# Performance work log

Measured on AMD Instinct MI355X. Metric: run time of the kernel, lower is better.

## Reference

```python
import jax, jax.numpy as jnp
import numpy as np

NUM_KERNELS = 5


def setup_inputs() -> dict:
    key = jax.random.key(0)
    k1, k2 = jax.random.split(key)
    B, D = 4096, 256
    return {
        "s_feat": jax.random.normal(k1, (B, D), dtype=jnp.float32),
        "t_feat": jax.random.normal(k2, (B, D), dtype=jnp.float32),
    }


def _pairwise_sq_dists(feats):
    # Gram-matrix form of sum((x_i - x_j)**2, axis=-1); same math as the
    # broadcasted (x - y)**2 sum, without the [N, N, D] intermediate.
    sq = jnp.sum(feats * feats, axis=-1)  # [N]
    d = sq[:, None] + sq[None, :] - 2.0 * (feats @ feats.T)  # [N, N]
    return jnp.maximum(d, 0.0)


def reference(s_feat, t_feat):
    batch = s_feat.shape[0]
    feats = jnp.concatenate((s_feat, t_feat), axis=0)  # [2B, D]
    distances = _pairwise_sq_dists(feats)  # [2B, 2B]

    # Median-heuristic-style bandwidth (detached in original).
    n = 2 * batch
    bandwidth = float(n * n - n) / jnp.sum(jax.lax.stop_gradient(distances))
    bandwidth = bandwidth / (2 ** (NUM_KERNELS // 2))
    gammas = [bandwidth * (2 ** i) for i in range(NUM_KERNELS)]

    # Multi-gamma Gaussian kernel average (fixed small loop over kernels).
    kern = sum(jnp.exp(-distances * g) for g in gammas) / NUM_KERNELS

    s2s = kern[:batch, :batch]
    t2t = kern[batch:, batch:]
    s2t = kern[:batch, batch:]
    disc = jnp.mean(s2s + t2t - 2.0 * s2t)
    return disc
```

## Files before the change

### kernel.cpp

```cpp
#include <hip/hip_runtime.h>
#include <stdint.h>
#include <math.h>

#define BATCH 4096
#define NT    8192
#define FD    256
#define TILE  128
#define BK    32
#define NUMK  5

typedef __attribute__((ext_vector_type(8))) short bf16x8;
typedef __attribute__((ext_vector_type(4))) float f32x4;

static const size_t WS_FB    = 0;
static const size_t WS_SQ    = (size_t)NT * FD * 2;
static const size_t WS_COL   = WS_SQ + (size_t)NT * 4;
static const size_t WS_SUMSQ = WS_COL + 256 * 4;

__device__ __forceinline__ unsigned short f2bf_rne(float x) {
    unsigned u = __float_as_uint(x);
    unsigned r = (u + 0x7fffu + ((u >> 16) & 1u)) >> 16;
    return (unsigned short)r;
}

__device__ __forceinline__ void async_copy16(void* lds, const void* g) {
    __builtin_amdgcn_global_load_lds(
        (__attribute__((address_space(1))) void*)(void*)(const_cast<void*>(g)),
        (__attribute__((address_space(3))) void*)lds, 16, 0, 0);
}

__global__ void mmd_prep(const float* __restrict__ s_feat,
                         const float* __restrict__ t_feat,
                         unsigned short* __restrict__ fb,
                         float* __restrict__ sq,
                         float* __restrict__ colsum,
                         float* __restrict__ sumsq,
                         float* __restrict__ out) {
    __shared__ float cp[4][FD];
    if (blockIdx.x == 0 && threadIdx.x == 0) atomicExch(out, 0.0f);
    const int w    = threadIdx.x >> 6;
    const int lane = threadIdx.x & 63;
    float c0 = 0.f, c1 = 0.f, c2 = 0.f, c3 = 0.f;
    float wtot = 0.f;
    for (int t = 0; t < 8; ++t) {
        int row = blockIdx.x * 32 + w * 8 + t;
        const float* src = (row < BATCH) ? (s_feat + (size_t)row * FD)
                                         : (t_feat + (size_t)(row - BATCH) * FD);
        float4 v = ((const float4*)src)[lane];
        unsigned int u01 = (unsigned)f2bf_rne(v.x) | ((unsigned)f2bf_rne(v.y) << 16);
        unsigned int u23 = (unsigned)f2bf_rne(v.z) | ((unsigned)f2bf_rne(v.w) << 16);
        ((uint2*)(fb + (size_t)row * FD))[lane] = make_uint2(u01, u23);
        float ss = v.x * v.x + v.y * v.y + v.z * v.z + v.w * v.w;
        for (int off = 32; off; off >>= 1) ss += __shfl_down(ss, off);
        if (lane == 0) { sq[row] = ss; wtot += ss; }
        c0 += v.x; c1 += v.y; c2 += v.z; c3 += v.w;
    }
    if (lane == 0) atomicAdd(sumsq, wtot);
    cp[w][4 * lane + 0] = c0;
    cp[w][4 * lane + 1] = c1;
    cp[w][4 * lane + 2] = c2;
    cp[w][4 * lane + 3] = c3;
    __syncthreads();
    int t = threadIdx.x;
    float s = cp[0][t] + cp[1][t] + cp[2][t] + cp[3][t];
    atomicAdd(&colsum[t], s);
}

__global__ __launch_bounds__(256, 4) void mmd_main(
    const unsigned short* __restrict__ fb,
    const float* __restrict__ sq,
    const float* __restrict__ colsum,
    const float* __restrict__ sumsq,
    float* __restrict__ out) {
    const int bid = blockIdx.x;
    int r = (int)((sqrtf(8.0f * (float)bid + 1.0f) - 1.0f) * 0.5f);
    while ((r + 1) * (r + 2) / 2 <= bid) ++r;
    while (r * (r + 1) / 2 > bid) --r;
    const int bi = bid - r * (r + 1) / 2;
    const int bj = r;

    __shared__ __align__(16) unsigned short a_t[3][TILE * BK];
    __shared__ __align__(16) unsigned short b_t[3][TILE * BK];
    __shared__ float sqa[TILE], sqb[TILE];
    __shared__ float red[4];

    const int tid  = threadIdx.x;
    const int w    = tid >> 6, lane = tid & 63;
    const int wm   = w & 1, wn = w >> 1;
    const int quad = lane >> 4, m16 = lane & 15;
    const int lrow16 = lane >> 2;
    const int pslot  = lane & 3;

    const size_t rowA0 = (size_t)bi * TILE;
    const size_t rowB0 = (size_t)bj * TILE;

#define STAGE(buf, k0_) do {                                                   \
        _Pragma("unroll")                                                      \
        for (int q = 0; q < 2; ++q) {                                          \
            int rr = w * 32 + q * 16 + lrow16;                                 \
            int gcq = pslot ^ ((rr >> 1) & 3);                                 \
            async_copy16(&a_t[buf][(w * 32 + q * 16) * BK],                    \
                         fb + (rowA0 + rr) * FD + (k0_) + gcq * 8);            \
        }                                                                      \
        _Pragma("unroll")                                                      \
        for (int q = 0; q < 2; ++q) {                                          \
            int rr = w * 32 + q * 16 + lrow16;                                 \
            int gcq = pslot ^ ((rr >> 1) & 3);                                 \
            async_copy16(&b_t[buf][(w * 32 + q * 16) * BK],                    \
                         fb + (rowB0 + rr) * FD + (k0_) + gcq * 8);            \
        }                                                                      \
    } while (0)

    STAGE(0, 0);
    STAGE(1, BK);

    float4 c4 = ((const float4*)colsum)[lane];
    float cv = c4.x * c4.x + c4.y * c4.y + c4.z * c4.z + c4.w * c4.w;
    for (int off = 1; off < 64; off <<= 1) cv += __shfl_xor(cv, off);
    const float sumd = 2.0f * (float)NT * sumsq[0] - 2.0f * cv;
    const float n2n  = (float)((long long)NT * NT - NT);
    const float g0   = 0.25f * (n2n / sumd);

    if (tid < TILE) sqa[tid] = sq[bi * TILE + tid];
    else            sqb[tid - TILE] = sq[bj * TILE + (tid - TILE)];

    const f32x4 fzero = {0.f, 0.f, 0.f, 0.f};
    f32x4 acc[4][4];
#pragma unroll
    for (int a = 0; a < 4; ++a)
#pragma unroll
        for (int b = 0; b < 4; ++b) acc[a][b] = fzero;

    __syncthreads();

#pragma unroll
    for (int st = 0; st < 8; ++st) {
        if (st >= 2) {
            if (st == 7) asm volatile("s_waitcnt vmcnt(0)" ::: "memory");
            else         asm volatile("s_waitcnt vmcnt(4)" ::: "memory");
        }
        if (st > 0) {
            __builtin_amdgcn_s_barrier();
            __builtin_amdgcn_sched_barrier(0);
        }
        const int cur = st % 3;

        bf16x8 af[4], bf[4];
#pragma unroll
        for (int tm = 0; tm < 4; ++tm) {
            int row = wm * 64 + tm * 16 + m16;
            int p = quad ^ ((row >> 1) & 3);
            af[tm] = *(const bf16x8*)&a_t[cur][row * BK + p * 8];
        }
#pragma unroll
        for (int tn = 0; tn < 4; ++tn) {
            int row = wn * 64 + tn * 16 + m16;
            int p = quad ^ ((row >> 1) & 3);
            bf[tn] = *(const bf16x8*)&b_t[cur][row * BK + p * 8];
        }

        if (st < 6) STAGE((st + 2) % 3, (st + 2) * BK);

        __builtin_amdgcn_s_setprio(1);
#pragma unroll
        for (int tm = 0; tm < 4; ++tm)
#pragma unroll
            for (int tn = 0; tn < 4; ++tn)
                acc[tm][tn] = __builtin_amdgcn_mfma_f32_16x16x32_bf16(
                    af[tm], bf[tn], acc[tm][tn], 0, 0, 0);
        __builtin_amdgcn_s_setprio(0);
    }

    float lsum = 0.f;
#pragma unroll
    for (int tm = 0; tm < 4; ++tm) {
        const int i0 = wm * 64 + tm * 16 + quad * 4;
        float sqi0 = sqa[i0 + 0], sqi1 = sqa[i0 + 1], sqi2 = sqa[i0 + 2], sqi3 = sqa[i0 + 3];
#pragma unroll
        for (int tn = 0; tn < 4; ++tn) {
            const int j = wn * 64 + tn * 16 + m16;
            const float sqj = sqb[j];
            float sqi[4] = {sqi0, sqi1, sqi2, sqi3};
#pragma unroll
            for (int rr = 0; rr < 4; ++rr) {
                float d = fmaf(-2.f, acc[tm][tn][rr], sqi[rr] + sqj);
                d = fmaxf(d, 0.f);
                float e1 = __expf(-d * g0);
                float e2 = e1 * e1, e4 = e2 * e2, e8 = e4 * e4, e16 = e8 * e8;
                lsum += e1 + e2 + e4 + e8 + e16;
            }
        }
    }
    for (int off = 32; off; off >>= 1) lsum += __shfl_down(lsum, off);
    if (lane == 0) red[w] = lsum;
    __syncthreads();
    if (tid == 0) {
        float wgt;
        if (bi == bj) wgt = 1.f;
        else wgt = ((bi < 32) == (bj < 32)) ? 2.f : -2.f;
        float scale = wgt * (1.f / NUMK) * (1.f / 16777216.f);
        atomicAdd(out, (red[0] + red[1] + red[2] + red[3]) * scale);
    }
}

extern "C" void kernel_launch(void* const* d_in, const int* in_sizes, int n_in,
                              void* d_out, int out_size, void* d_ws, size_t ws_size,
                              hipStream_t stream) {
    const float* s_feat = (const float*)d_in[0];
    const float* t_feat = (const float*)d_in[1];
    char* ws = (char*)d_ws;
    unsigned short* fb = (unsigned short*)(ws + WS_FB);
    float* sq     = (float*)(ws + WS_SQ);
    float* colsum = (float*)(ws + WS_COL);
    float* sumsq  = (float*)(ws + WS_SUMSQ);
    float* out    = (float*)d_out;

    hipMemsetAsync(ws + WS_COL, 0, 256 * 4 + 4, stream);

    mmd_prep<<<NT / 32, 256, 0, stream>>>(s_feat, t_feat, fb, sq, colsum, sumsq, out);
    mmd_main<<<2080, 256, 0, stream>>>(fb, sq, colsum, sumsq, out);
}
```

Before: 119.7 us.

## Deepen LDS pipeline to four stages and swizzle block order across XCDs

Moves the main tile loop from a three-buffer to a four-buffer async global-to-LDS pipeline, prefetching three K-steps ahead and adjusting the vmcnt waits to match. Block IDs are remapped so consecutive blocks spread across the eight XCDs, aiming to improve L2 reuse of shared row tiles. The sq and colsum loads are issued earlier to hide their latency, and the epilogue reduction is split into four accumulators to shorten the dependency chain. Launch bounds drop to 2 blocks per SM, which frees more registers but may reduce occupancy, and the extra LDS buffer raises shared memory use.

```diff
diff --git a/kernel.cpp b/kernel.cpp
--- a/kernel.cpp
+++ b/kernel.cpp
@@ -8,6 +8,7 @@
 #define TILE  128
 #define BK    32
 #define NUMK  5
+#define NTRI  2080
 
 typedef __attribute__((ext_vector_type(8))) short bf16x8;
 typedef __attribute__((ext_vector_type(4))) float f32x4;
@@ -66,21 +67,22 @@
     atomicAdd(&colsum[t], s);
 }
 
-__global__ __launch_bounds__(256, 4) void mmd_main(
+__global__ __launch_bounds__(256, 2) void mmd_main(
     const unsigned short* __restrict__ fb,
     const float* __restrict__ sq,
     const float* __restrict__ colsum,
     const float* __restrict__ sumsq,
     float* __restrict__ out) {
     const int bid = blockIdx.x;
-    int r = (int)((sqrtf(8.0f * (float)bid + 1.0f) - 1.0f) * 0.5f);
-    while ((r + 1) * (r + 2) / 2 <= bid) ++r;
-    while (r * (r + 1) / 2 > bid) --r;
-    const int bi = bid - r * (r + 1) / 2;
+    const int swz = (bid & 7) * (NTRI / 8) + (bid >> 3);
+    int r = (int)((sqrtf(8.0f * (float)swz + 1.0f) - 1.0f) * 0.5f);
+    while ((r + 1) * (r + 2) / 2 <= swz) ++r;
+    while (r * (r + 1) / 2 > swz) --r;
+    const int bi = swz - r * (r + 1) / 2;
     const int bj = r;
 
-    __shared__ __align__(16) unsigned short a_t[3][TILE * BK];
-    __shared__ __align__(16) unsigned short b_t[3][TILE * BK];
+    __shared__ __align__(16) unsigned short a_t[4][TILE * BK];
+    __shared__ __align__(16) unsigned short b_t[4][TILE * BK];
     __shared__ float sqa[TILE], sqb[TILE];
     __shared__ float red[4];
 
@@ -93,6 +95,9 @@
 
     const size_t rowA0 = (size_t)bi * TILE;
     const size_t rowB0 = (size_t)bj * TILE;
+
+    const float sqv = (tid < TILE) ? sq[rowA0 + tid] : sq[rowB0 + (tid - TILE)];
+    float4 c4 = ((const float4*)colsum)[lane];
 
 #define STAGE(buf, k0_) do {                                                   \
         _Pragma("unroll")                                                      \
@@ -113,16 +118,16 @@
 
     STAGE(0, 0);
     STAGE(1, BK);
-
-    float4 c4 = ((const float4*)colsum)[lane];
+    STAGE(2, 2 * BK);
+
     float cv = c4.x * c4.x + c4.y * c4.y + c4.z * c4.z + c4.w * c4.w;
     for (int off = 1; off < 64; off <<= 1) cv += __shfl_xor(cv, off);
     const float sumd = 2.0f * (float)NT * sumsq[0] - 2.0f * cv;
     const float n2n  = (float)((long long)NT * NT - NT);
     const float g0   = 0.25f * (n2n / sumd);
 
-    if (tid < TILE) sqa[tid] = sq[bi * TILE + tid];
-    else            sqb[tid - TILE] = sq[bj * TILE + (tid - TILE)];
+    if (tid < TILE) sqa[tid] = sqv;
+    else            sqb[tid - TILE] = sqv;
 
     const f32x4 fzero = {0.f, 0.f, 0.f, 0.f};
     f32x4 acc[4][4];
@@ -135,15 +140,14 @@
 
 #pragma unroll
     for (int st = 0; st < 8; ++st) {
-        if (st >= 2) {
-            if (st == 7) asm volatile("s_waitcnt vmcnt(0)" ::: "memory");
-            else         asm volatile("s_waitcnt vmcnt(4)" ::: "memory");
-        }
         if (st > 0) {
+            if (st <= 5)      asm volatile("s_waitcnt vmcnt(8)" ::: "memory");
+            else if (st == 6) asm volatile("s_waitcnt vmcnt(4)" ::: "memory");
+            else              asm volatile("s_waitcnt vmcnt(0)" ::: "memory");
             __builtin_amdgcn_s_barrier();
             __builtin_amdgcn_sched_barrier(0);
         }
-        const int cur = st % 3;
+        const int cur = st & 3;
 
         bf16x8 af[4], bf[4];
 #pragma unroll
@@ -159,7 +163,8 @@
             bf[tn] = *(const bf16x8*)&b_t[cur][row * BK + p * 8];
         }
 
-        if (st < 6) STAGE((st + 2) % 3, (st + 2) * BK);
+        if (st < 5) STAGE((st + 3) & 3, (st + 3) * BK);
+        __builtin_amdgcn_sched_barrier(0);
 
         __builtin_amdgcn_s_setprio(1);
 #pragma unroll
@@ -171,7 +176,7 @@
         __builtin_amdgcn_s_setprio(0);
     }
 
-    float lsum = 0.f;
+    float ls[4] = {0.f, 0.f, 0.f, 0.f};
 #pragma unroll
     for (int tm = 0; tm < 4; ++tm) {
         const int i0 = wm * 64 + tm * 16 + quad * 4;
@@ -187,10 +192,11 @@
                 d = fmaxf(d, 0.f);
                 float e1 = __expf(-d * g0);
                 float e2 = e1 * e1, e4 = e2 * e2, e8 = e4 * e4, e16 = e8 * e8;
-                lsum += e1 + e2 + e4 + e8 + e16;
+                ls[rr] += e1 + e2 + e4 + e8 + e16;
             }
         }
     }
+    float lsum = (ls[0] + ls[1]) + (ls[2] + ls[3]);
     for (int off = 32; off; off >>= 1) lsum += __shfl_down(lsum, off);
     if (lane == 0) red[w] = lsum;
     __syncthreads();
@@ -218,5 +224,5 @@
     hipMemsetAsync(ws + WS_COL, 0, 256 * 4 + 4, stream);
 
     mmd_prep<<<NT / 32, 256, 0, stream>>>(s_feat, t_feat, fb, sq, colsum, sumsq, out);
-    mmd_main<<<2080, 256, 0, stream>>>(fb, sq, colsum, sumsq, out);
-}
+    mmd_main<<<NTRI, 256, 0, stream>>>(fb, sq, colsum, sumsq, out);
+}
```

Result: slower. 122.8 us (+2.5%).

## Use 256x128 rectangular tiles with 512 threads over the upper triangle

Applied to the files above, without the earlier changes.

Replaces the 128x128 upper-triangular tile scheme with 256x128 tiles processed by 512-thread blocks, so each A tile is reused across eight waves and the block count roughly halves. Tiles that straddle the diagonal apply per-element weights (2, 1 or 0) to avoid double counting. It also deepens the prefetch to three stages before the loop, moves the async copies to just after the barrier, and swizzles block order for L2 locality. In exchange, straddling tiles compute some wasted entries, and the larger blocks may reduce occupancy.

```diff
diff --git a/kernel.cpp b/kernel.cpp
--- a/kernel.cpp
+++ b/kernel.cpp
@@ -5,9 +5,11 @@
 #define BATCH 4096
 #define NT    8192
 #define FD    256
-#define TILE  128
+#define TM    256
+#define TN    128
 #define BK    32
 #define NUMK  5
+#define NBLK  1056
 
 typedef __attribute__((ext_vector_type(8))) short bf16x8;
 typedef __attribute__((ext_vector_type(4))) float f32x4;
@@ -66,63 +68,69 @@
     atomicAdd(&colsum[t], s);
 }
 
-__global__ __launch_bounds__(256, 4) void mmd_main(
+__global__ __launch_bounds__(512, 4) void mmd_main(
     const unsigned short* __restrict__ fb,
     const float* __restrict__ sq,
     const float* __restrict__ colsum,
     const float* __restrict__ sumsq,
     float* __restrict__ out) {
     const int bid = blockIdx.x;
-    int r = (int)((sqrtf(8.0f * (float)bid + 1.0f) - 1.0f) * 0.5f);
-    while ((r + 1) * (r + 2) / 2 <= bid) ++r;
-    while (r * (r + 1) / 2 > bid) --r;
-    const int bi = bid - r * (r + 1) / 2;
-    const int bj = r;
-
-    __shared__ __align__(16) unsigned short a_t[3][TILE * BK];
-    __shared__ __align__(16) unsigned short b_t[3][TILE * BK];
-    __shared__ float sqa[TILE], sqb[TILE];
-    __shared__ float red[4];
+    const int swz = (bid & 7) * (NBLK / 8) + (bid >> 3);
+    int I = (int)((65.0f - sqrtf(fmaxf(4225.0f - 4.0f * (float)swz, 0.f))) * 0.5f);
+    if (I > 31) I = 31;
+    while (I > 0 && I * (65 - I) > swz) --I;
+    while (I < 31 && (I + 1) * (65 - (I + 1)) <= swz) ++I;
+    const int J = 2 * I + (swz - I * (65 - I));
+    const bool straddle = ((J >> 1) == I);
+
+    __shared__ __align__(16) unsigned short a_t[3][TM * BK];
+    __shared__ __align__(16) unsigned short b_t[3][TN * BK];
+    __shared__ float sqa[TM], sqb[TN];
+    __shared__ float red[8];
 
     const int tid  = threadIdx.x;
     const int w    = tid >> 6, lane = tid & 63;
-    const int wm   = w & 1, wn = w >> 1;
+    const int wm2  = w >> 1, wn2 = w & 1;
     const int quad = lane >> 4, m16 = lane & 15;
     const int lrow16 = lane >> 2;
     const int pslot  = lane & 3;
 
-    const size_t rowA0 = (size_t)bi * TILE;
-    const size_t rowB0 = (size_t)bj * TILE;
+    const size_t rowA0 = (size_t)I * TM;
+    const size_t rowB0 = (size_t)J * TN;
+
+    float sqv = 0.f;
+    if (tid < TM)                sqv = sq[rowA0 + tid];
+    else if (tid < TM + TN)      sqv = sq[rowB0 + (tid - TM)];
+    float4 c4 = ((const float4*)colsum)[lane];
 
 #define STAGE(buf, k0_) do {                                                   \
         _Pragma("unroll")                                                      \
         for (int q = 0; q < 2; ++q) {                                          \
-            int rr = w * 32 + q * 16 + lrow16;                                 \
-            int gcq = pslot ^ ((rr >> 1) & 3);                                 \
+            int rr_ = w * 32 + q * 16 + lrow16;                    \
+            int gc_ = pslot ^ ((rr_ >> 1) & 3);                                \
             async_copy16(&a_t[buf][(w * 32 + q * 16) * BK],                    \
-                         fb + (rowA0 + rr) * FD + (k0_) + gcq * 8);            \
+                         fb + (rowA0 + rr_) * FD + (k0_) + gc_ * 8);           \
         }                                                                      \
-        _Pragma("unroll")                                                      \
-        for (int q = 0; q < 2; ++q) {                                          \
-            int rr = w * 32 + q * 16 + lrow16;                                 \
-            int gcq = pslot ^ ((rr >> 1) & 3);                                 \
-            async_copy16(&b_t[buf][(w * 32 + q * 16) * BK],                    \
-                         fb + (rowB0 + rr) * FD + (k0_) + gcq * 8);            \
+        {                                                                      \
+            int rr_ = w * 16 + lrow16;                             \
+            int gc_ = pslot ^ ((rr_ >> 1) & 3);                                \
+            async_copy16(&b_t[buf][(w * 16) * BK],                             \
+                         fb + (rowB0 + rr_) * FD + (k0_) + gc_ * 8);           \
         }                                                                      \
     } while (0)
 
     STAGE(0, 0);
     STAGE(1, BK);
-
-    float4 c4 = ((const float4*)colsum)[lane];
+    STAGE(2, 2 * BK);
+
     float cv = c4.x * c4.x + c4.y * c4.y + c4.z * c4.z + c4.w * c4.w;
     for (int off = 1; off < 64; off <<= 1) cv += __shfl_xor(cv, off);
     const float sumd = 2.0f * (float)NT * sumsq[0] - 2.0f * cv;
     const float n2n  = (float)((long long)NT * NT - NT);
     const float g0   = 0.25f * (n2n / sumd);
 
-    if (tid < TILE) sqa[tid] = sq[bi * TILE + tid];
-    else            sqb[tid - TILE] = sq[bj * TILE + (tid - TILE)];
+    if (tid < TM)                sqa[tid] = sqv;
+    else if (tid < TM + TN)      sqb[tid - TM] = sqv;
 
     const f32x4 fzero = {0.f, 0.f, 0.f, 0.f};
     f32x4 acc[4][4];
@@ -135,31 +143,31 @@
 
 #pragma unroll
     for (int st = 0; st < 8; ++st) {
-        if (st >= 2) {
-            if (st == 7) asm volatile("s_waitcnt vmcnt(0)" ::: "memory");
-            else         asm volatile("s_waitcnt vmcnt(4)" ::: "memory");
-        }
         if (st > 0) {
+            if (st >= 3) {
+                if (st == 7) asm volatile("s_waitcnt vmcnt(0)" ::: "memory");
+                else         asm volatile("s_waitcnt vmcnt(3)" ::: "memory");
+            }
             __builtin_amdgcn_s_barrier();
             __builtin_amdgcn_sched_barrier(0);
+            if (st <= 5) STAGE((st + 2) % 3, (st + 2) * BK);
         }
         const int cur = st % 3;
 
         bf16x8 af[4], bf[4];
 #pragma unroll
         for (int tm = 0; tm < 4; ++tm) {
-            int row = wm * 64 + tm * 16 + m16;
+            int row = wm2 * 64 + tm * 16 + m16;
             int p = quad ^ ((row >> 1) & 3);
             af[tm] = *(const bf16x8*)&a_t[cur][row * BK + p * 8];
         }
 #pragma unroll
         for (int tn = 0; tn < 4; ++tn) {
-            int row = wn * 64 + tn * 16 + m16;
+            int row = wn2 * 64 + tn * 16 + m16;
             int p = quad ^ ((row >> 1) & 3);
             bf[tn] = *(const bf16x8*)&b_t[cur][row * BK + p * 8];
         }
-
-        if (st < 6) STAGE((st + 2) % 3, (st + 2) * BK);
+        __builtin_amdgcn_sched_barrier(0);
 
         __builtin_amdgcn_s_setprio(1);
 #pragma unroll
@@ -171,35 +179,62 @@
         __builtin_amdgcn_s_setprio(0);
     }
 
-    float lsum = 0.f;
-#pragma unroll
-    for (int tm = 0; tm < 4; ++tm) {
-        const int i0 = wm * 64 + tm * 16 + quad * 4;
-        float sqi0 = sqa[i0 + 0], sqi1 = sqa[i0 + 1], sqi2 = sqa[i0 + 2], sqi3 = sqa[i0 + 3];
-#pragma unroll
-        for (int tn = 0; tn < 4; ++tn) {
-            const int j = wn * 64 + tn * 16 + m16;
-            const float sqj = sqb[j];
-            float sqi[4] = {sqi0, sqi1, sqi2, sqi3};
-#pragma unroll
-            for (int rr = 0; rr < 4; ++rr) {
-                float d = fmaf(-2.f, acc[tm][tn][rr], sqi[rr] + sqj);
-                d = fmaxf(d, 0.f);
-                float e1 = __expf(-d * g0);
-                float e2 = e1 * e1, e4 = e2 * e2, e8 = e4 * e4, e16 = e8 * e8;
-                lsum += e1 + e2 + e4 + e8 + e16;
+    float ls[4] = {0.f, 0.f, 0.f, 0.f};
+    if (!straddle) {
+#pragma unroll
+        for (int tm = 0; tm < 4; ++tm) {
+            const int i0 = wm2 * 64 + tm * 16 + quad * 4;
+            float sqi[4] = {sqa[i0 + 0], sqa[i0 + 1], sqa[i0 + 2], sqa[i0 + 3]};
+#pragma unroll
+            for (int tn = 0; tn < 4; ++tn) {
+                const int j = wn2 * 64 + tn * 16 + m16;
+                const float sqj = sqb[j];
+#pragma unroll
+                for (int rr = 0; rr < 4; ++rr) {
+                    float d = fmaf(-2.f, acc[tm][tn][rr], sqi[rr] + sqj);
+                    d = fmaxf(d, 0.f);
+                    float e1 = __expf(-d * g0);
+                    float e2 = e1 * e1, e4 = e2 * e2, e8 = e4 * e4, e16 = e8 * e8;
+                    ls[rr] += e1 + e2 + e4 + e8 + e16;
+                }
             }
         }
-    }
+    } else {
+        const int dOff = (J - 2 * I) * TN;
+#pragma unroll
+        for (int tm = 0; tm < 4; ++tm) {
+            const int i0 = wm2 * 64 + tm * 16 + quad * 4;
+            float sqi[4] = {sqa[i0 + 0], sqa[i0 + 1], sqa[i0 + 2], sqa[i0 + 3]};
+#pragma unroll
+            for (int tn = 0; tn < 4; ++tn) {
+                const int j = wn2 * 64 + tn * 16 + m16;
+                const float sqj = sqb[j];
+                const int jg = j + dOff;
+#pragma unroll
+                for (int rr = 0; rr < 4; ++rr) {
+                    const int ig = i0 + rr;
+                    float wf = (jg > ig) ? 2.f : ((jg == ig) ? 1.f : 0.f);
+                    float d = fmaf(-2.f, acc[tm][tn][rr], sqi[rr] + sqj);
+                    d = fmaxf(d, 0.f);
+                    float e1 = __expf(-d * g0);
+                    float e2 = e1 * e1, e4 = e2 * e2, e8 = e4 * e4, e16 = e8 * e8;
+                    ls[rr] += wf * (e1 + e2 + e4 + e8 + e16);
+                }
+            }
+        }
+    }
+    float lsum = (ls[0] + ls[1]) + (ls[2] + ls[3]);
     for (int off = 32; off; off >>= 1) lsum += __shfl_down(lsum, off);
     if (lane == 0) red[w] = lsum;
     __syncthreads();
     if (tid == 0) {
         float wgt;
-        if (bi == bj) wgt = 1.f;
-        else wgt = ((bi < 32) == (bj < 32)) ? 2.f : -2.f;
+        if (straddle) wgt = 1.f;
+        else wgt = ((I < 16) == (J < 32)) ? 2.f : -2.f;
         float scale = wgt * (1.f / NUMK) * (1.f / 16777216.f);
-        atomicAdd(out, (red[0] + red[1] + red[2] + red[3]) * scale);
+        float tot = ((red[0] + red[1]) + (red[2] + red[3]))
+                  + ((red[4] + red[5]) + (red[6] + red[7]));
+        atomicAdd(out, tot * scale);
     }
 }
 
@@ -218,5 +253,5 @@
     hipMemsetAsync(ws + WS_COL, 0, 256 * 4 + 4, stream);
 
     mmd_prep<<<NT / 32, 256, 0, stream>>>(s_feat, t_feat, fb, sq, colsum, sumsq, out);
-    mmd_main<<<2080, 256, 0, stream>>>(fb, sq, colsum, sumsq, out);
-}
+    mmd_main<<<NBLK, 512, 0, stream>>>(fb, sq, colsum, sumsq, out);
+}
```

Result: faster. 115.0 us (-4.0%).
